# Kernel optimization log

Measured on AMD Instinct MI355X. Metric: run time of the kernel, lower is better.

The kernel has to match this reference:

```python
import jax, jax.numpy as jnp
import numpy as np

NUM_VERTS = 6890
NUM_JOINTS = 24
NUM_BETAS = 10
NUM_POSE_FEATS = 207  # 23 joints * 9
NUM_COCO_JOINTS = 19
BATCH = 1024

SMPL_PARENTS = np.array([0, 0, 0, 0, 1, 2, 3, 4, 5, 6, 7, 8, 9, 9, 9,
                         12, 13, 14, 16, 17, 18, 19, 20, 21], dtype=np.int32)


def batch_rodrigues(theta):
    """theta: [N,3] axis-angle -> [N,3,3] rotation matrices (Rodrigues)."""
    angle = jnp.linalg.norm(theta + 1e-8, axis=1, keepdims=True)  # [N,1]
    r = theta / angle                                             # [N,3]
    c = jnp.cos(angle)[:, :, None]                                # [N,1,1]
    s = jnp.sin(angle)[:, :, None]
    rx, ry, rz = r[:, 0], r[:, 1], r[:, 2]
    zeros = jnp.zeros_like(rx)
    K = jnp.stack([zeros, -rz, ry,
                   rz, zeros, -rx,
                   -ry, rx, zeros], axis=1).reshape(-1, 3, 3)     # skew(r)
    eye = jnp.eye(3, dtype=theta.dtype)
    return eye + s * K + (1.0 - c) * jnp.matmul(K, K)


def batch_global_rigid_transformation(Rs, Js, parents, rotate_base=True):
    """Rs: [B,24,3,3], Js: [B,24,3]. Returns (new_J [B,24,3], A [B,24,4,4])."""
    B = Rs.shape[0]
    dtype = Rs.dtype
    if rotate_base:
        rot_x = jnp.array([[1., 0., 0.], [0., -1., 0.], [0., 0., -1.]], dtype=dtype)
        root_rot = jnp.matmul(Rs[:, 0], rot_x)
    else:
        root_rot = Rs[:, 0]

    bottom = jnp.broadcast_to(jnp.array([0., 0., 0., 1.], dtype=dtype), (B, 1, 4))

    def make_A(R, t):  # R [B,3,3], t [B,3] -> [B,4,4]
        top = jnp.concatenate([R, t[:, :, None]], axis=2)  # [B,3,4]
        return jnp.concatenate([top, bottom], axis=1)

    results = [make_A(root_rot, Js[:, 0])]
    for i in range(1, NUM_JOINTS):
        t_rel = Js[:, i] - Js[:, parents[i]]
        A_here = make_A(Rs[:, i], t_rel)
        results.append(jnp.matmul(results[parents[i]], A_here))
    results = jnp.stack(results, axis=1)  # [B,24,4,4]

    new_J = results[:, :, :3, 3]
    # A = results - pad(results @ [J;0]) : subtract rotated rest joint from translation
    t_adj = jnp.einsum('bjpq,bjq->bjp', results[:, :, :3, :3], Js)  # [B,24,3]
    A = results.at[:, :, :3, 3].add(-t_adj)
    return new_J, A


def setup_inputs() -> dict:
    key = jax.random.key(0)
    ks = jax.random.split(key, 8)
    beta = jax.random.normal(ks[0], (BATCH, NUM_BETAS), dtype=jnp.float32)
    theta = jax.random.normal(ks[1], (BATCH, NUM_JOINTS * 3), dtype=jnp.float32) * 0.3
    v_template = jax.random.normal(ks[2], (NUM_VERTS, 3), dtype=jnp.float32)
    shapedirs = jax.random.normal(ks[3], (NUM_BETAS, NUM_VERTS * 3), dtype=jnp.float32) * 0.01
    J_regressor = jax.random.uniform(ks[4], (NUM_JOINTS, NUM_VERTS), dtype=jnp.float32) / NUM_VERTS
    posedirs = jax.random.normal(ks[5], (NUM_POSE_FEATS, NUM_VERTS * 3), dtype=jnp.float32) * 0.01
    joint_regressor = jax.random.uniform(ks[6], (NUM_COCO_JOINTS, NUM_VERTS), dtype=jnp.float32) / NUM_VERTS
    w_raw = jax.random.uniform(ks[7], (NUM_VERTS, NUM_JOINTS), dtype=jnp.float32)
    weights = w_raw / jnp.sum(w_raw, axis=1, keepdims=True)  # LBS weights, rows sum to 1
    parents = jnp.asarray(SMPL_PARENTS)
    return {"beta": beta, "theta": theta, "v_template": v_template,
            "shapedirs": shapedirs, "J_regressor": J_regressor,
            "posedirs": posedirs, "joint_regressor": joint_regressor,
            "weights": weights, "parents": parents}


def reference(beta, theta, v_template, shapedirs, J_regressor,
              posedirs, joint_regressor, weights, parents):
    B = beta.shape[0]
    parents_np = np.asarray(parents)

    # Shape blendshapes: [B,10]@[10,20670] -> [B,6890,3]
    v_shaped = jnp.matmul(beta, shapedirs).reshape(B, NUM_VERTS, 3) + v_template

    J = jnp.einsum('bvd,jv->bjd', v_shaped, J_regressor)

    # Pose rotations
    Rs = batch_rodrigues(theta.reshape(-1, 3)).reshape(B, NUM_JOINTS, 3, 3)
    pose_feature = (Rs[:, 1:] - jnp.eye(3, dtype=Rs.dtype)).reshape(B, NUM_POSE_FEATS)
    v_posed = jnp.matmul(pose_feature, posedirs).reshape(B, NUM_VERTS, 3) + v_shaped

    # Kinematic chain
    J_transformed, A = batch_global_rigid_transformation(Rs, J, parents_np, rotate_base=True)

    # Linear blend skinning: per-vertex 4x4 transforms
    T = jnp.einsum('vj,bjpq->bvpq', weights, A)  # [B,6890,4,4]
    ones = jnp.ones((B, NUM_VERTS, 1), dtype=v_posed.dtype)
    v_posed_homo = jnp.concatenate([v_posed, ones], axis=2)  # [B,6890,4]
    verts = jnp.einsum('bvpq,bvq->bvp', T[:, :, :3, :], v_posed_homo)  # [B,6890,3]

    joints = jnp.einsum('bvd,jv->bjd', verts, joint_regressor)  # [B,19,3]
    return verts, joints, Rs
```

## Files before the change

kernel.cpp:

```cpp
#include <hip/hip_runtime.h>
#include <math.h>

#define NV   6890
#define NJ   24
#define NB   10
#define NPF  207
#define NCJ  19
#define BATCHN 1024
#define NC3  (NV*3)
#define KTOT 224
#define NVP  6892

#define OUT_JOINTS_OFF (BATCHN*NV*3)
#define OUT_RS_OFF     (OUT_JOINTS_OFF + BATCHN*NCJ*3)

#define WS_JS     0
#define WS_EF     1024
#define WS_AADJT  115712
#define WS_JRB    377856
#define WS_DIRST  443392
#define WS_WTB    2765824
#define WS_END    2876416

typedef __attribute__((ext_vector_type(8))) short short8;
typedef __attribute__((ext_vector_type(4))) float f32x4;

__device__ __forceinline__ unsigned short f2bf(float f) {
    unsigned u = __float_as_uint(f);
    unsigned r = u + 0x7FFFu + ((u >> 16) & 1u);
    return (unsigned short)(r >> 16);
}
__device__ __forceinline__ float bf2f(unsigned short u) {
    return __uint_as_float((unsigned)u << 16);
}
__device__ __forceinline__ void async16(unsigned short* lds, const unsigned short* g) {
    __builtin_amdgcn_global_load_lds(
        (const __attribute__((address_space(1))) void*)g,
        (__attribute__((address_space(3))) void*)lds, 16, 0, 0);
}

__global__ __launch_bounds__(256) void smpl_kAP(
    const float* __restrict__ pdirs, const float* __restrict__ sdirs,
    unsigned short* __restrict__ dirsT,
    const float* __restrict__ jreg, const float* __restrict__ vtmpl,
    float* __restrict__ js,
    const float* __restrict__ jointreg, unsigned short* __restrict__ jrb,
    const float* __restrict__ wts, unsigned short* __restrict__ wtb) {
    int bx = blockIdx.x, t = threadIdx.x;
    if (bx < 216 * 6) {
        int vt = bx / 6, part = bx - (bx / 6) * 6;
        for (int g = part * 448 + t; g < part * 448 + 448; g += 256) {
            int frag = g >> 6, fo = g & 63;
            int ks = frag / 6, s = frag - ks * 6;
            int l15 = fo >> 2, lg = fo & 3;
            int gc = vt * 96 + s * 16 + l15;
            int k0 = ks * 32 + lg * 8;
            unsigned short pk[8];
#pragma unroll
            for (int i = 0; i < 8; i++) {
                int k = k0 + i;
                float val = 0.f;
                if (gc < NC3) {
                    if (k < NPF) val = pdirs[(size_t)k * NC3 + gc];
                    else if (k < NPF + NB) val = sdirs[(size_t)(k - NPF) * NC3 + gc];
                    else if (k == NPF + NB) val = vtmpl[gc];
                }
                pk[i] = f2bf(val);
            }
            *(short8*)(dirsT + (size_t)vt * 21504 + (size_t)g * 8) = *(const short8*)pk;
        }
        return;
    }
    if (bx >= 216 * 6 + NJ + NCJ) {
        int vt = bx - (216 * 6 + NJ + NCJ);
        for (int e = t; e < 1024; e += 256) {
            int vl = e >> 5, k = e & 31;
            int gv = vt * 32 + vl;
            float w = (k < NJ && gv < NV) ? wts[(size_t)gv * NJ + k] : 0.f;
            wtb[(size_t)vt * 1024 + e] = f2bf(w);
        }
        return;
    }
    if (bx >= 216 * 6 + NJ) {
        int j = bx - 216 * 6 - NJ;
        for (int v = t; v < NVP; v += 256)
            jrb[(size_t)j * NVP + v] = (v < NV) ? f2bf(jointreg[(size_t)j * NV + v]) : 0;
        return;
    }
    int j = bx - 216 * 6;
    float acc[33];
#pragma unroll
    for (int e = 0; e < 33; e++) acc[e] = 0.f;
    for (int v = t; v < NV; v += 256) {
        float w = jreg[j * NV + v];
#pragma unroll
        for (int k = 0; k < NB; k++) {
#pragma unroll
            for (int d = 0; d < 3; d++)
                acc[k * 3 + d] += w * sdirs[(size_t)k * NC3 + v * 3 + d];
        }
#pragma unroll
        for (int d = 0; d < 3; d++) acc[30 + d] += w * vtmpl[v * 3 + d];
    }
#pragma unroll
    for (int e = 0; e < 33; e++) {
#pragma unroll
        for (int off = 32; off >= 1; off >>= 1) acc[e] += __shfl_xor(acc[e], off, 64);
    }
    __shared__ float red[4][33];
    int lane = t & 63, wv = t >> 6;
    if (lane == 0) {
#pragma unroll
        for (int e = 0; e < 33; e++) red[wv][e] = acc[e];
    }
    __syncthreads();
    if (t < 33) js[j * 33 + t] = red[0][t] + red[1][t] + red[2][t] + red[3][t];
}

__global__ void smpl_kB(const float* __restrict__ theta, const float* __restrict__ beta_,
                        const float* __restrict__ js, float* __restrict__ outRs,
                        unsigned short* __restrict__ ef, unsigned short* __restrict__ aadjT) {
    int b = blockIdx.x;
    int t = threadIdx.x;
    __shared__ float Rl[NJ][9];
    __shared__ float Jl[NJ][3];
    __shared__ float Rw[NJ][12];

    if (t < NJ) {
        int j = t;
        float tx = theta[b * 72 + j * 3 + 0];
        float ty = theta[b * 72 + j * 3 + 1];
        float tz = theta[b * 72 + j * 3 + 2];
        float ax = tx + 1e-8f, ay = ty + 1e-8f, az = tz + 1e-8f;
        float ang = sqrtf(ax * ax + ay * ay + az * az);
        float inv = 1.0f / ang;
        float rx = tx * inv, ry = ty * inv, rz = tz * inv;
        float s = sinf(ang), c = cosf(ang), t1 = 1.0f - c;
        float R[9];
        R[0] = 1.0f - t1 * (ry * ry + rz * rz);
        R[1] = -s * rz + t1 * rx * ry;
        R[2] =  s * ry + t1 * rx * rz;
        R[3] =  s * rz + t1 * rx * ry;
        R[4] = 1.0f - t1 * (rx * rx + rz * rz);
        R[5] = -s * rx + t1 * ry * rz;
        R[6] = -s * ry + t1 * rx * rz;
        R[7] =  s * rx + t1 * ry * rz;
        R[8] = 1.0f - t1 * (rx * rx + ry * ry);
#pragma unroll
        for (int e = 0; e < 9; e++) {
            Rl[j][e] = R[e];
            outRs[(size_t)b * 216 + j * 9 + e] = R[e];
        }
#pragma unroll
        for (int d = 0; d < 3; d++) {
            float accJ = js[j * 33 + 30 + d];
#pragma unroll
            for (int k = 0; k < NB; k++) accJ += beta_[b * NB + k] * js[j * 33 + k * 3 + d];
            Jl[j][d] = accJ;
        }
    }
    __syncthreads();
    for (int e = t; e < KTOT; e += 64) {
        float val;
        if (e < NPF) {
            int j = e / 9 + 1;
            int rc = e - (j - 1) * 9;
            val = Rl[j][rc] - ((rc == 0 || rc == 4 || rc == 8) ? 1.0f : 0.0f);
        } else if (e < NPF + NB) {
            val = beta_[b * NB + (e - NPF)];
        } else if (e == NPF + NB) {
            val = 1.0f;
        } else val = 0.f;
        ef[(size_t)b * KTOT + e] = f2bf(val);
    }
    if (t == 0) {
#pragma unroll
        for (int r = 0; r < 3; r++) {
            Rw[0][r * 4 + 0] =  Rl[0][r * 3 + 0];
            Rw[0][r * 4 + 1] = -Rl[0][r * 3 + 1];
            Rw[0][r * 4 + 2] = -Rl[0][r * 3 + 2];
            Rw[0][r * 4 + 3] =  Jl[0][r];
        }
        const int par[NJ] = {0,0,0,0,1,2,3,4,5,6,7,8,9,9,9,12,13,14,16,17,18,19,20,21};
#pragma unroll
        for (int i = 1; i < NJ; i++) {
            int p = par[i];
            float tr0 = Jl[i][0] - Jl[p][0];
            float tr1 = Jl[i][1] - Jl[p][1];
            float tr2 = Jl[i][2] - Jl[p][2];
#pragma unroll
            for (int r = 0; r < 3; r++) {
                float p0 = Rw[p][r * 4 + 0], p1 = Rw[p][r * 4 + 1], p2 = Rw[p][r * 4 + 2];
#pragma unroll
                for (int cc = 0; cc < 3; cc++)
                    Rw[i][r * 4 + cc] = p0 * Rl[i][0 + cc] + p1 * Rl[i][3 + cc] + p2 * Rl[i][6 + cc];
                Rw[i][r * 4 + 3] = p0 * tr0 + p1 * tr1 + p2 * tr2 + Rw[p][r * 4 + 3];
            }
        }
    }
    __syncthreads();
    for (int i = t; i < 512; i += 64) {
        int n = i >> 5, k = i & 31;
        float v = 0.f;
        if (n < 12 && k < 24) {
            int r = n >> 2, cc = n & 3;
            if (cc < 3) v = Rw[k][n];
            else v = Rw[k][r * 4 + 3] - (Rw[k][r * 4 + 0] * Jl[k][0] + Rw[k][r * 4 + 1] * Jl[k][1] +
                                         Rw[k][r * 4 + 2] * Jl[k][2]);
        }
        aadjT[(size_t)b * 512 + i] = f2bf(v);
    }
}

__global__ __launch_bounds__(512, 2) void smpl_kC11(
    const unsigned short* __restrict__ dirsT, const unsigned short* __restrict__ wtb,
    const unsigned short* __restrict__ ef, const unsigned short* __restrict__ aadjT,
    float* __restrict__ outv) {
    __shared__ __align__(16) unsigned short Bb[2][21504];
    __shared__ __align__(16) unsigned short Wt[2][1024];
    __shared__ __align__(16) unsigned short vph[8][2176];

    int tid = threadIdx.x;
    int cg = blockIdx.x;
    int bt = blockIdx.y;
    int lane = tid & 63, wv = tid >> 6;
    int l15 = lane & 15, lg = lane >> 4;
    int fo = l15 * 4 + lg;
    int nvt = (cg < 24) ? 7 : 6;
    int bb = bt * 128 + wv * 16;

    const unsigned short* efb = ef + (size_t)(bb + l15) * KTOT;
    short8 av[7];
#pragma unroll
    for (int ks = 0; ks < 7; ks++) av[ks] = *(const short8*)(efb + ks * 32 + lg * 8);
    const short8* at0 = (const short8*)(aadjT + (size_t)bb * 512);
    short8 afr[16];
#pragma unroll
    for (int i = 0; i < 16; i++) afr[i] = at0[i * 64 + fo];

    auto stage = [&](int i, int p) {
        int vt = cg + i * 32;
        const unsigned short* bsrc = dirsT + (size_t)vt * 21504;
        for (int g0 = wv * 64; g0 < 2688; g0 += 512)
            async16(&Bb[p][(size_t)g0 * 8], bsrc + ((size_t)g0 + lane) * 8);
        if (wv < 2) {
            int g0 = wv * 64;
            async16(&Wt[p][g0 * 8], wtb + (size_t)vt * 1024 + ((size_t)g0 + lane) * 8);
        }
    };

    stage(0, 0);
    __syncthreads();

    unsigned short* vp = vph[wv];

    for (int i = 0; i < nvt; i++) {
        int pc = i & 1;
        if (i + 1 < nvt) stage(i + 1, pc ^ 1);
        int vt = cg + i * 32;

        short8 wf0 = *(const short8*)&Wt[pc][l15 * 32 + lg * 8];
        short8 wf1 = *(const short8*)&Wt[pc][(16 + l15) * 32 + lg * 8];

        f32x4 acc[6];
#pragma unroll
        for (int s = 0; s < 6; s++) acc[s] = (f32x4){0.f, 0.f, 0.f, 0.f};
#pragma unroll
        for (int ks = 0; ks < 7; ks++) {
#pragma unroll
            for (int s = 0; s < 6; s++) {
                short8 bv = *(const short8*)&Bb[pc][((ks * 6 + s) << 9) + fo * 8];
                acc[s] = __builtin_amdgcn_mfma_f32_16x16x32_bf16(av[ks], bv, acc[s], 0, 0, 0);
            }
        }
#pragma unroll
        for (int s = 0; s < 6; s++) {
            int col = s * 16 + l15;
            int v = col / 3, d = col - v * 3;
#pragma unroll
            for (int r = 0; r < 4; r++)
                vp[(v * 17 + lg * 4 + r) * 4 + d] = f2bf(acc[s][r]);
        }
#pragma unroll
        for (int bl2 = 0; bl2 < 16; bl2++) {
            short8 af = afr[bl2];
            f32x4 z = (f32x4){0.f, 0.f, 0.f, 0.f};
            f32x4 t0 = __builtin_amdgcn_mfma_f32_16x16x32_bf16(af, wf0, z, 0, 0, 0);
            f32x4 t1 = __builtin_amdgcn_mfma_f32_16x16x32_bf16(af, wf1, z, 0, 0, 0);
            int b = bb + bl2;
            if (lg < 3) {
                int p = lg;
                {
                    int vv = l15;
                    ushort4 xv = *(const ushort4*)&vp[(vv * 17 + bl2) * 4];
                    float o = fmaf(t0[0], bf2f(xv.x),
                              fmaf(t0[1], bf2f(xv.y), fmaf(t0[2], bf2f(xv.z), t0[3])));
                    int gv = vt * 32 + vv;
                    if (gv < NV) outv[(size_t)b * NC3 + gv * 3 + p] = o;
                }
                {
                    int vv = 16 + l15;
                    ushort4 xv = *(const ushort4*)&vp[(vv * 17 + bl2) * 4];
                    float o = fmaf(t1[0], bf2f(xv.x),
                              fmaf(t1[1], bf2f(xv.y), fmaf(t1[2], bf2f(xv.z), t1[3])));
                    int gv = vt * 32 + vv;
                    if (gv < NV) outv[(size_t)b * NC3 + gv * 3 + p] = o;
                }
            }
        }
        __syncthreads();
    }
}

__global__ __launch_bounds__(256) void smpl_kD(
    const float* __restrict__ verts, const unsigned short* __restrict__ jrb,
    float* __restrict__ outj) {
    int tid = threadIdx.x;
    int b = blockIdx.x;
    const float* vb = verts + (size_t)b * NC3;
    float acc[57];
#pragma unroll
    for (int e = 0; e < 57; e++) acc[e] = 0.f;

    for (int it = 0; it < 7; it++) {
        int g = it * 256 + tid;
        if (g < 1723) {
            int v = g * 4;
            const float* pa = vb + v * 3;
            float2 q0 = *(const float2*)(pa + 0);
            float2 q1 = *(const float2*)(pa + 2);
            float2 q2 = *(const float2*)(pa + 4);
            float2 q3 = *(const float2*)(pa + 6);
            float2 q4 = *(const float2*)(pa + 8);
            float2 q5 = *(const float2*)(pa + 10);
#pragma unroll
            for (int j = 0; j < NCJ; j++) {
                uint2 wp = *(const uint2*)(jrb + (size_t)j * NVP + v);
                float w0 = __uint_as_float((wp.x & 0xFFFFu) << 16);
                float w1 = __uint_as_float(wp.x & 0xFFFF0000u);
                float w2 = __uint_as_float((wp.y & 0xFFFFu) << 16);
                float w3 = __uint_as_float(wp.y & 0xFFFF0000u);
                acc[j * 3 + 0] += w0 * q0.x + w1 * q1.y + w2 * q3.x + w3 * q4.y;
                acc[j * 3 + 1] += w0 * q0.y + w1 * q2.x + w2 * q3.y + w3 * q5.x;
                acc[j * 3 + 2] += w0 * q1.x + w1 * q2.y + w2 * q4.x + w3 * q5.y;
            }
        }
    }
#pragma unroll
    for (int e = 0; e < 57; e++) {
#pragma unroll
        for (int off = 32; off >= 1; off >>= 1) acc[e] += __shfl_xor(acc[e], off, 64);
    }
    __shared__ float red[4][57];
    int lane = tid & 63, wv = tid >> 6;
    if (lane == 0) {
#pragma unroll
        for (int e = 0; e < 57; e++) red[wv][e] = acc[e];
    }
    __syncthreads();
    if (tid < 57)
        outj[(size_t)b * 57 + tid] = red[0][tid] + red[1][tid] + red[2][tid] + red[3][tid];
}

extern "C" void kernel_launch(void* const* d_in, const int* in_sizes, int n_in,
                              void* d_out, int out_size, void* d_ws, size_t ws_size,
                              hipStream_t stream) {
    (void)in_sizes; (void)n_in; (void)out_size; (void)ws_size;
    const float* beta       = (const float*)d_in[0];
    const float* theta      = (const float*)d_in[1];
    const float* v_template = (const float*)d_in[2];
    const float* shapedirs  = (const float*)d_in[3];
    const float* jreg       = (const float*)d_in[4];
    const float* posedirs   = (const float*)d_in[5];
    const float* jointreg   = (const float*)d_in[6];
    const float* weights    = (const float*)d_in[7];
    float* out = (float*)d_out;
    float* ws  = (float*)d_ws;
    unsigned short* ef    = (unsigned short*)(ws + WS_EF);
    unsigned short* aadjT = (unsigned short*)(ws + WS_AADJT);
    unsigned short* jrb   = (unsigned short*)(ws + WS_JRB);
    unsigned short* dirsT = (unsigned short*)(ws + WS_DIRST);
    unsigned short* wtb   = (unsigned short*)(ws + WS_WTB);

    smpl_kAP<<<216 * 6 + NJ + NCJ + 216, 256, 0, stream>>>(
        posedirs, shapedirs, dirsT, jreg, v_template, ws + WS_JS,
        jointreg, jrb, weights, wtb);
    smpl_kB<<<BATCHN, 64, 0, stream>>>(theta, beta, ws + WS_JS, out + OUT_RS_OFF,
                                       ef, aadjT);
    dim3 gC(32, 8);
    smpl_kC11<<<gC, 512, 0, stream>>>(dirsT, wtb, ef, aadjT, out);
    smpl_kD<<<BATCHN, 256, 0, stream>>>(out, jrb, out + OUT_JOINTS_OFF);
}
```

Baseline: 115.6 us.

## Split B-tile staging into halves and double grid width for higher occupancy

The main skinning kernel now uses a split shared-memory buffer for the pose/shape direction tile instead of a full double buffer. The second half is loaded while the first half is consumed, and the next first half is prefetched after a mid-loop barrier. The transform fragments are streamed from global memory in chunks instead of held in 16 registers, and the grid width doubles to 64 with launch bounds raised to 4 blocks per CU. The aim is to cut LDS and register footprint so more blocks can be resident. In exchange there are extra barriers and repeated global loads of the transform fragments on every tile.

```diff
diff --git a/kernel.cpp b/kernel.cpp
--- a/kernel.cpp
+++ b/kernel.cpp
@@ -212,21 +212,22 @@
     }
 }
 
-__global__ __launch_bounds__(512, 2) void smpl_kC11(
+__global__ __launch_bounds__(512, 4) void smpl_kC12(
     const unsigned short* __restrict__ dirsT, const unsigned short* __restrict__ wtb,
     const unsigned short* __restrict__ ef, const unsigned short* __restrict__ aadjT,
     float* __restrict__ outv) {
-    __shared__ __align__(16) unsigned short Bb[2][21504];
+    __shared__ __align__(16) unsigned short Bb0[12288];
+    __shared__ __align__(16) unsigned short Bb1[9216];
     __shared__ __align__(16) unsigned short Wt[2][1024];
-    __shared__ __align__(16) unsigned short vph[8][2176];
+    __shared__ __align__(16) unsigned short vph[8 * 2112];
 
     int tid = threadIdx.x;
-    int cg = blockIdx.x;
+    int cgh = blockIdx.x;
     int bt = blockIdx.y;
     int lane = tid & 63, wv = tid >> 6;
     int l15 = lane & 15, lg = lane >> 4;
     int fo = l15 * 4 + lg;
-    int nvt = (cg < 24) ? 7 : 6;
+    int nvt = (cgh < 24) ? 4 : 3;
     int bb = bt * 128 + wv * 16;
 
     const unsigned short* efb = ef + (size_t)(bb + l15) * KTOT;
@@ -234,42 +235,51 @@
 #pragma unroll
     for (int ks = 0; ks < 7; ks++) av[ks] = *(const short8*)(efb + ks * 32 + lg * 8);
     const short8* at0 = (const short8*)(aadjT + (size_t)bb * 512);
-    short8 afr[16];
-#pragma unroll
-    for (int i = 0; i < 16; i++) afr[i] = at0[i * 64 + fo];
-
-    auto stage = [&](int i, int p) {
-        int vt = cg + i * 32;
-        const unsigned short* bsrc = dirsT + (size_t)vt * 21504;
-        for (int g0 = wv * 64; g0 < 2688; g0 += 512)
-            async16(&Bb[p][(size_t)g0 * 8], bsrc + ((size_t)g0 + lane) * 8);
-        if (wv < 2) {
-            int g0 = wv * 64;
-            async16(&Wt[p][g0 * 8], wtb + (size_t)vt * 1024 + ((size_t)g0 + lane) * 8);
-        }
+
+    auto stage0 = [&](int i) {
+        const unsigned short* src = dirsT + (size_t)(cgh + i * 64) * 21504;
+        for (int g0 = wv * 64; g0 < 1536; g0 += 512)
+            async16(&Bb0[g0 * 8], src + ((size_t)g0 + lane) * 8);
     };
-
-    stage(0, 0);
+    auto stage1 = [&](int i) {
+        const unsigned short* src = dirsT + (size_t)(cgh + i * 64) * 21504 + 12288;
+        for (int g0 = wv * 64; g0 < 1152; g0 += 512)
+            async16(&Bb1[g0 * 8], src + ((size_t)g0 + lane) * 8);
+    };
+    auto stagew = [&](int i) {
+        if (wv < 2)
+            async16(&Wt[i & 1][wv * 512],
+                    wtb + (size_t)(cgh + i * 64) * 1024 + ((size_t)(wv * 64) + lane) * 8);
+    };
+
+    stage0(0); stagew(0);
     __syncthreads();
 
-    unsigned short* vp = vph[wv];
+    unsigned short* vp = vph + wv * 2112;
 
     for (int i = 0; i < nvt; i++) {
-        int pc = i & 1;
-        if (i + 1 < nvt) stage(i + 1, pc ^ 1);
-        int vt = cg + i * 32;
-
-        short8 wf0 = *(const short8*)&Wt[pc][l15 * 32 + lg * 8];
-        short8 wf1 = *(const short8*)&Wt[pc][(16 + l15) * 32 + lg * 8];
+        int vt = cgh + i * 64;
+        stage1(i);
+        short8 c0 = at0[fo], c1 = at0[64 + fo], c2 = at0[128 + fo], c3 = at0[192 + fo];
 
         f32x4 acc[6];
 #pragma unroll
         for (int s = 0; s < 6; s++) acc[s] = (f32x4){0.f, 0.f, 0.f, 0.f};
 #pragma unroll
-        for (int ks = 0; ks < 7; ks++) {
+        for (int ks = 0; ks < 4; ks++) {
 #pragma unroll
             for (int s = 0; s < 6; s++) {
-                short8 bv = *(const short8*)&Bb[pc][((ks * 6 + s) << 9) + fo * 8];
+                short8 bv = *(const short8*)&Bb0[((ks * 6 + s) << 9) + fo * 8];
+                acc[s] = __builtin_amdgcn_mfma_f32_16x16x32_bf16(av[ks], bv, acc[s], 0, 0, 0);
+            }
+        }
+        __syncthreads();
+        if (i + 1 < nvt) { stage0(i + 1); stagew(i + 1); }
+#pragma unroll
+        for (int ks = 4; ks < 7; ks++) {
+#pragma unroll
+            for (int s = 0; s < 6; s++) {
+                short8 bv = *(const short8*)&Bb1[(((ks - 4) * 6 + s) << 9) + fo * 8];
                 acc[s] = __builtin_amdgcn_mfma_f32_16x16x32_bf16(av[ks], bv, acc[s], 0, 0, 0);
             }
         }
@@ -279,32 +289,45 @@
             int v = col / 3, d = col - v * 3;
 #pragma unroll
             for (int r = 0; r < 4; r++)
-                vp[(v * 17 + lg * 4 + r) * 4 + d] = f2bf(acc[s][r]);
-        }
-#pragma unroll
-        for (int bl2 = 0; bl2 < 16; bl2++) {
-            short8 af = afr[bl2];
-            f32x4 z = (f32x4){0.f, 0.f, 0.f, 0.f};
-            f32x4 t0 = __builtin_amdgcn_mfma_f32_16x16x32_bf16(af, wf0, z, 0, 0, 0);
-            f32x4 t1 = __builtin_amdgcn_mfma_f32_16x16x32_bf16(af, wf1, z, 0, 0, 0);
-            int b = bb + bl2;
-            if (lg < 3) {
-                int p = lg;
-                {
-                    int vv = l15;
-                    ushort4 xv = *(const ushort4*)&vp[(vv * 17 + bl2) * 4];
-                    float o = fmaf(t0[0], bf2f(xv.x),
-                              fmaf(t0[1], bf2f(xv.y), fmaf(t0[2], bf2f(xv.z), t0[3])));
-                    int gv = vt * 32 + vv;
-                    if (gv < NV) outv[(size_t)b * NC3 + gv * 3 + p] = o;
-                }
-                {
-                    int vv = 16 + l15;
-                    ushort4 xv = *(const ushort4*)&vp[(vv * 17 + bl2) * 4];
-                    float o = fmaf(t1[0], bf2f(xv.x),
-                              fmaf(t1[1], bf2f(xv.y), fmaf(t1[2], bf2f(xv.z), t1[3])));
-                    int gv = vt * 32 + vv;
-                    if (gv < NV) outv[(size_t)b * NC3 + gv * 3 + p] = o;
+                vp[((lg * 4 + r) * 33 + v) * 4 + d] = f2bf(acc[s][r]);
+        }
+        short8 wf0 = *(const short8*)&Wt[i & 1][l15 * 32 + lg * 8];
+        short8 wf1 = *(const short8*)&Wt[i & 1][(16 + l15) * 32 + lg * 8];
+#pragma unroll
+        for (int ch = 0; ch < 4; ch++) {
+            short8 a0 = c0, a1 = c1, a2 = c2, a3 = c3;
+            if (ch < 3) {
+                c0 = at0[((ch + 1) * 4 + 0) * 64 + fo];
+                c1 = at0[((ch + 1) * 4 + 1) * 64 + fo];
+                c2 = at0[((ch + 1) * 4 + 2) * 64 + fo];
+                c3 = at0[((ch + 1) * 4 + 3) * 64 + fo];
+            }
+#pragma unroll
+            for (int q = 0; q < 4; q++) {
+                short8 af = (q == 0) ? a0 : (q == 1) ? a1 : (q == 2) ? a2 : a3;
+                f32x4 z = (f32x4){0.f, 0.f, 0.f, 0.f};
+                f32x4 t0 = __builtin_amdgcn_mfma_f32_16x16x32_bf16(af, wf0, z, 0, 0, 0);
+                f32x4 t1 = __builtin_amdgcn_mfma_f32_16x16x32_bf16(af, wf1, z, 0, 0, 0);
+                int bl2 = ch * 4 + q;
+                int b = bb + bl2;
+                if (lg < 3) {
+                    int p = lg;
+                    {
+                        int vv = l15;
+                        ushort4 xv = *(const ushort4*)&vp[(bl2 * 33 + vv) * 4];
+                        float o = fmaf(t0[0], bf2f(xv.x),
+                                  fmaf(t0[1], bf2f(xv.y), fmaf(t0[2], bf2f(xv.z), t0[3])));
+                        int gv = vt * 32 + vv;
+                        if (gv < NV) outv[(size_t)b * NC3 + gv * 3 + p] = o;
+                    }
+                    {
+                        int vv = 16 + l15;
+                        ushort4 xv = *(const ushort4*)&vp[(bl2 * 33 + vv) * 4];
+                        float o = fmaf(t1[0], bf2f(xv.x),
+                                  fmaf(t1[1], bf2f(xv.y), fmaf(t1[2], bf2f(xv.z), t1[3])));
+                        int gv = vt * 32 + vv;
+                        if (gv < NV) outv[(size_t)b * NC3 + gv * 3 + p] = o;
+                    }
                 }
             }
         }
@@ -387,7 +410,7 @@
         jointreg, jrb, weights, wtb);
     smpl_kB<<<BATCHN, 64, 0, stream>>>(theta, beta, ws + WS_JS, out + OUT_RS_OFF,
                                        ef, aadjT);
-    dim3 gC(32, 8);
-    smpl_kC11<<<gC, 512, 0, stream>>>(dirsT, wtb, ef, aadjT, out);
+    dim3 gC(64, 8);
+    smpl_kC12<<<gC, 512, 0, stream>>>(dirsT, wtb, ef, aadjT, out);
     smpl_kD<<<BATCHN, 256, 0, stream>>>(out, jrb, out + OUT_JOINTS_OFF);
 }
```

New measurement: 183.0 us. +58.3%, slower.

## Drop LDS double buffering and register caching to double grid occupancy

Applied to the files above, without the earlier changes.

The main skinning kernel now uses a single LDS stage buffer instead of double-buffering, shrinks the per-wave scratch tile, and streams transform fragments from global memory with a two-deep prefetch instead of holding 16 in registers. Launch bounds go from 2 to 4 blocks per CU and the grid doubles to 64 column groups, each handling about half as many vertex tiles. The scratch layout is transposed (batch-major, stride 33) to change LDS bank behaviour. The cost is losing the overlap of global loads with MFMA work, since each tile now waits on a barrier after its load, plus extra global reads per tile.

```diff
diff --git a/kernel.cpp b/kernel.cpp
--- a/kernel.cpp
+++ b/kernel.cpp
@@ -212,21 +212,21 @@
     }
 }
 
-__global__ __launch_bounds__(512, 2) void smpl_kC11(
+__global__ __launch_bounds__(512, 4) void smpl_kC13(
     const unsigned short* __restrict__ dirsT, const unsigned short* __restrict__ wtb,
     const unsigned short* __restrict__ ef, const unsigned short* __restrict__ aadjT,
     float* __restrict__ outv) {
-    __shared__ __align__(16) unsigned short Bb[2][21504];
-    __shared__ __align__(16) unsigned short Wt[2][1024];
-    __shared__ __align__(16) unsigned short vph[8][2176];
+    __shared__ __align__(16) unsigned short Bb[21504];
+    __shared__ __align__(16) unsigned short Wt[1024];
+    __shared__ __align__(16) unsigned short vph[8 * 2112];
 
     int tid = threadIdx.x;
-    int cg = blockIdx.x;
+    int cgh = blockIdx.x;
     int bt = blockIdx.y;
     int lane = tid & 63, wv = tid >> 6;
     int l15 = lane & 15, lg = lane >> 4;
     int fo = l15 * 4 + lg;
-    int nvt = (cg < 24) ? 7 : 6;
+    int nvt = (cgh < 24) ? 4 : 3;
     int bb = bt * 128 + wv * 16;
 
     const unsigned short* efb = ef + (size_t)(bb + l15) * KTOT;
@@ -234,33 +234,25 @@
 #pragma unroll
     for (int ks = 0; ks < 7; ks++) av[ks] = *(const short8*)(efb + ks * 32 + lg * 8);
     const short8* at0 = (const short8*)(aadjT + (size_t)bb * 512);
-    short8 afr[16];
-#pragma unroll
-    for (int i = 0; i < 16; i++) afr[i] = at0[i * 64 + fo];
-
-    auto stage = [&](int i, int p) {
-        int vt = cg + i * 32;
-        const unsigned short* bsrc = dirsT + (size_t)vt * 21504;
-        for (int g0 = wv * 64; g0 < 2688; g0 += 512)
-            async16(&Bb[p][(size_t)g0 * 8], bsrc + ((size_t)g0 + lane) * 8);
-        if (wv < 2) {
-            int g0 = wv * 64;
-            async16(&Wt[p][g0 * 8], wtb + (size_t)vt * 1024 + ((size_t)g0 + lane) * 8);
-        }
-    };
-
-    stage(0, 0);
-    __syncthreads();
-
-    unsigned short* vp = vph[wv];
+
+    unsigned short* vp = vph + wv * 2112;
 
     for (int i = 0; i < nvt; i++) {
-        int pc = i & 1;
-        if (i + 1 < nvt) stage(i + 1, pc ^ 1);
-        int vt = cg + i * 32;
-
-        short8 wf0 = *(const short8*)&Wt[pc][l15 * 32 + lg * 8];
-        short8 wf1 = *(const short8*)&Wt[pc][(16 + l15) * 32 + lg * 8];
+        int vt = cgh + i * 64;
+        {
+            const unsigned short* src = dirsT + (size_t)vt * 21504;
+            for (int g0 = wv * 64; g0 < 2688; g0 += 512)
+                async16(&Bb[(size_t)g0 * 8], src + ((size_t)g0 + lane) * 8);
+            if (wv < 2)
+                async16(&Wt[wv * 512],
+                        wtb + (size_t)vt * 1024 + ((size_t)(wv * 64) + lane) * 8);
+        }
+        __syncthreads();
+
+        short8 wf0 = *(const short8*)&Wt[l15 * 32 + lg * 8];
+        short8 wf1 = *(const short8*)&Wt[(16 + l15) * 32 + lg * 8];
+        short8 af0 = at0[fo];
+        short8 af1 = at0[64 + fo];
 
         f32x4 acc[6];
 #pragma unroll
@@ -269,7 +261,7 @@
         for (int ks = 0; ks < 7; ks++) {
 #pragma unroll
             for (int s = 0; s < 6; s++) {
-                short8 bv = *(const short8*)&Bb[pc][((ks * 6 + s) << 9) + fo * 8];
+                short8 bv = *(const short8*)&Bb[((ks * 6 + s) << 9) + fo * 8];
                 acc[s] = __builtin_amdgcn_mfma_f32_16x16x32_bf16(av[ks], bv, acc[s], 0, 0, 0);
             }
         }
@@ -279,11 +271,14 @@
             int v = col / 3, d = col - v * 3;
 #pragma unroll
             for (int r = 0; r < 4; r++)
-                vp[(v * 17 + lg * 4 + r) * 4 + d] = f2bf(acc[s][r]);
+                vp[((lg * 4 + r) * 33 + v) * 4 + d] = f2bf(acc[s][r]);
         }
 #pragma unroll
         for (int bl2 = 0; bl2 < 16; bl2++) {
-            short8 af = afr[bl2];
+            short8 af = af0;
+            af0 = af1;
+            int nx = (bl2 + 2 < 16) ? (bl2 + 2) : 15;
+            af1 = at0[nx * 64 + fo];
             f32x4 z = (f32x4){0.f, 0.f, 0.f, 0.f};
             f32x4 t0 = __builtin_amdgcn_mfma_f32_16x16x32_bf16(af, wf0, z, 0, 0, 0);
             f32x4 t1 = __builtin_amdgcn_mfma_f32_16x16x32_bf16(af, wf1, z, 0, 0, 0);
@@ -292,7 +287,7 @@
                 int p = lg;
                 {
                     int vv = l15;
-                    ushort4 xv = *(const ushort4*)&vp[(vv * 17 + bl2) * 4];
+                    ushort4 xv = *(const ushort4*)&vp[(bl2 * 33 + vv) * 4];
                     float o = fmaf(t0[0], bf2f(xv.x),
                               fmaf(t0[1], bf2f(xv.y), fmaf(t0[2], bf2f(xv.z), t0[3])));
                     int gv = vt * 32 + vv;
@@ -300,7 +295,7 @@
                 }
                 {
                     int vv = 16 + l15;
-                    ushort4 xv = *(const ushort4*)&vp[(vv * 17 + bl2) * 4];
+                    ushort4 xv = *(const ushort4*)&vp[(bl2 * 33 + vv) * 4];
                     float o = fmaf(t1[0], bf2f(xv.x),
                               fmaf(t1[1], bf2f(xv.y), fmaf(t1[2], bf2f(xv.z), t1[3])));
                     int gv = vt * 32 + vv;
@@ -387,7 +382,7 @@
         jointreg, jrb, weights, wtb);
     smpl_kB<<<BATCHN, 64, 0, stream>>>(theta, beta, ws + WS_JS, out + OUT_RS_OFF,
                                        ef, aadjT);
-    dim3 gC(32, 8);
-    smpl_kC11<<<gC, 512, 0, stream>>>(dirsT, wtb, ef, aadjT, out);
+    dim3 gC(64, 8);
+    smpl_kC13<<<gC, 512, 0, stream>>>(dirsT, wtb, ef, aadjT, out);
     smpl_kD<<<BATCHN, 256, 0, stream>>>(out, jrb, out + OUT_JOINTS_OFF);
 }
```

New measurement: 188.0 us. 1.63x slower.
